# Performance work log

Measured on AMD Instinct MI355X. Metric: run time of the kernel, lower is better.

The kernel has to match this reference:

```python
import jax, jax.numpy as jnp
import numpy as np

B, S, D = 1, 8192, 1024
H, HD = 16, 64
WIN = 1024      # sliding_window_size
CHUNK = 1024    # chunk_size
OVERLAP = 128   # chunk_overlap


def setup_inputs() -> dict:
    key = jax.random.key(0)
    ks = jax.random.split(key, 5)
    s = 1.0 / np.sqrt(D)
    inp = {"x": jax.random.normal(ks[0], (B, S, D), jnp.float32)}
    for i, n in enumerate(["Wq", "Wk", "Wv", "Wo"]):
        inp[n] = jax.random.normal(ks[1 + i], (D, D), jnp.float32) * s
    for n in ["bq", "bk", "bv", "bo"]:
        inp[n] = jnp.zeros((D,), jnp.float32)
    return inp


def _attend_chunk(q, k, v, chunk_start, win_start):
    # q: [B, Lq, H, HD]; k, v: [B, Lk, H, HD]
    Lq, Lk = q.shape[1], k.shape[1]
    q_abs = chunk_start + jnp.arange(Lq)[:, None]   # absolute query positions
    k_abs = win_start + jnp.arange(Lk)[None, :]     # absolute key positions
    allowed = (k_abs >= q_abs - WIN // 2) & (k_abs < q_abs + WIN // 2)
    scale = 1.0 / np.sqrt(HD)
    scores = jnp.einsum('bqhd,bkhd->bhqk', q, k) * scale  # [B,H,Lq,Lk]
    scores = jnp.where(allowed[None, None], scores, -jnp.inf)
    p = jax.nn.softmax(scores, axis=-1)
    return jnp.einsum('bhqk,bkhd->bqhd', p, v)


def _overlap_weight(cs, ce):
    # replicate torch linspace overlap-add blend weights (host-side constants)
    w = np.ones(ce - cs, np.float32)
    if cs > 0:
        n = min(cs + OVERLAP, ce) - cs
        w[:n] = np.linspace(0.0, 1.0, n, dtype=np.float32)
    if ce < S:
        os_ = max(cs, ce - OVERLAP)
        w[os_ - cs:] = np.linspace(1.0, 0.0, ce - os_, dtype=np.float32)
    return jnp.asarray(w)


def reference(x, Wq, bq, Wk, bk, Wv, bv, Wo, bo):
    q = (x @ Wq.T + bq).reshape(B, S, H, HD)
    k = (x @ Wk.T + bk).reshape(B, S, H, HD)
    v = (x @ Wv.T + bv).reshape(B, S, H, HD)
    out = jnp.zeros((B, S, H, HD), x.dtype)
    step = CHUNK - OVERLAP
    for cs in range(0, S, step):  # static Python loop over ~10 chunks
        ce = min(cs + CHUNK, S)
        ws, we = max(0, cs - WIN // 2), min(S, ce + WIN // 2)
        o = _attend_chunk(q[:, cs:ce], k[:, ws:we], v[:, ws:we], cs, ws)
        w = _overlap_weight(cs, ce)
        out = out.at[:, cs:ce].add(o * w[None, :, None, None])
    out = out.reshape(B, S, D)
    return out @ Wo.T + bo
```

## Files before the change

### kernel.cpp

```cpp
#include <hip/hip_runtime.h>

#define DEVI __device__ __forceinline__

constexpr int S = 8192, D = 1024, H = 16, HD = 64;
constexpr int NQKV = 3 * D;

typedef __attribute__((ext_vector_type(8))) __bf16 bf16x8;
typedef __attribute__((ext_vector_type(8))) unsigned short us8;
typedef __attribute__((ext_vector_type(4))) float f32x4;

DEVI unsigned short f2b(float f) {
  unsigned int u = __float_as_uint(f);
  u += 0x7fff + ((u >> 16) & 1);
  return (unsigned short)(u >> 16);
}

DEVI ushort4 cvt4(float4 v) {
  ushort4 r; r.x = f2b(v.x); r.y = f2b(v.y); r.z = f2b(v.z); r.w = f2b(v.w); return r;
}

DEVI void load_lds16(const void* g, void* l) {
  __builtin_amdgcn_global_load_lds((const __attribute__((address_space(1))) void*)g,
                                   (__attribute__((address_space(3))) void*)l,
                                   16, 0, 0);
}

__global__ void prep_kernel(const float4* __restrict__ x,
                            const float4* __restrict__ Wq, const float4* __restrict__ Wk,
                            const float4* __restrict__ Wv, const float4* __restrict__ Wo,
                            const float4* __restrict__ bq, const float4* __restrict__ bk,
                            const float4* __restrict__ bv,
                            ushort4* __restrict__ xb, ushort4* __restrict__ wqkv,
                            ushort4* __restrict__ wob, float4* __restrict__ biasq)
{
  constexpr int NX = S * D / 4;
  constexpr int NW = D * D / 4;
  constexpr int NB = D / 4;
  constexpr int TOT = NX + 4 * NW + 3 * NB;
  for (int i = blockIdx.x * blockDim.x + threadIdx.x; i < TOT; i += gridDim.x * blockDim.x) {
    if (i < NX) {
      xb[i] = cvt4(x[i]);
    } else if (i < NX + 3 * NW) {
      int j = i - NX;
      const float4* src = (j < NW) ? Wq : ((j < 2 * NW) ? Wk : Wv);
      int jj = (j < NW) ? j : ((j < 2 * NW) ? j - NW : j - 2 * NW);
      wqkv[j] = cvt4(src[jj]);
    } else if (i < NX + 4 * NW) {
      int j = i - NX - 3 * NW;
      wob[j] = cvt4(Wo[j]);
    } else {
      int j = i - NX - 4 * NW;
      const float4* src = (j < NB) ? bq : ((j < 2 * NB) ? bk : bv);
      int jj = (j < NB) ? j : ((j < 2 * NB) ? j - NB : j - 2 * NB);
      biasq[j] = src[jj];
    }
  }
}

template<int LDC, bool OUT_BF16>
__global__ __launch_bounds__(256)
void gemm_nt(const unsigned short* __restrict__ A,
             const unsigned short* __restrict__ B,
             const float* __restrict__ bias,
             void* __restrict__ C, int K)
{
  __shared__ __align__(16) unsigned short As[128 * 32];
  __shared__ __align__(16) unsigned short Bs[128 * 32];
  const int tid = threadIdx.x;
  const int wave = tid >> 6, lane = tid & 63;
  const int quad = lane >> 4, l15 = lane & 15;
  const int m0 = blockIdx.x * 128, n0 = blockIdx.y * 128;
  const int wr = wave >> 1, wc = wave & 1;

  const f32x4 fzero = {0.f, 0.f, 0.f, 0.f};
  f32x4 acc[4][4];
#pragma unroll
  for (int i = 0; i < 4; ++i)
#pragma unroll
    for (int j = 0; j < 4; ++j) acc[i][j] = fzero;

  const int segr = lane >> 2;
  const int cpst = lane & 3;

  for (int k0 = 0; k0 < K; k0 += 32) {
    __syncthreads();
#pragma unroll
    for (int j = 0; j < 4; ++j) {
      const int s = wave * 4 + j;
      const int s7 = s & 7;
      const int r = s7 * 16 + segr;
      const int c = cpst ^ ((r >> 1) & 3);
      const unsigned short* g = (s < 8)
        ? A + (size_t)(m0 + r) * K + k0 + c * 8
        : B + (size_t)(n0 + r) * K + k0 + c * 8;
      unsigned short* l = ((s < 8) ? As : Bs) + s7 * 512;
      load_lds16(g, l);
    }
    __syncthreads();

    bf16x8 af[4], bfr[4];
#pragma unroll
    for (int it = 0; it < 4; ++it) {
      const int r = wr * 64 + it * 16 + l15;
      const int cp = quad ^ ((r >> 1) & 3);
      af[it] = *(const bf16x8*)&As[r * 32 + cp * 8];
    }
#pragma unroll
    for (int jt = 0; jt < 4; ++jt) {
      const int r = wc * 64 + jt * 16 + l15;
      const int cp = quad ^ ((r >> 1) & 3);
      bfr[jt] = *(const bf16x8*)&Bs[r * 32 + cp * 8];
    }
#pragma unroll
    for (int it = 0; it < 4; ++it)
#pragma unroll
      for (int jt = 0; jt < 4; ++jt)
        acc[it][jt] = __builtin_amdgcn_mfma_f32_16x16x32_bf16(af[it], bfr[jt], acc[it][jt], 0, 0, 0);
  }

#pragma unroll
  for (int it = 0; it < 4; ++it)
#pragma unroll
    for (int jt = 0; jt < 4; ++jt) {
      const int col = n0 + wc * 64 + jt * 16 + l15;
      const float bv = bias[col];
#pragma unroll
      for (int i = 0; i < 4; ++i) {
        const int row = m0 + wr * 64 + it * 16 + quad * 4 + i;
        const float v = acc[it][jt][i] + bv;
        if constexpr (OUT_BF16)
          ((unsigned short*)C)[(size_t)row * LDC + col] = f2b(v);
        else
          ((float*)C)[(size_t)row * LDC + col] = v;
      }
    }
}

__global__ __launch_bounds__(256)
void attn_fused(const unsigned short* __restrict__ qkv,
                unsigned short* __restrict__ attnb)
{
  __shared__ __align__(16) unsigned short Ks[64 * 64];
  __shared__ __align__(16) unsigned short Vt[64 * 72];
  __shared__ __align__(16) unsigned short Ps[4][2][16 * 72];
  const int tid = threadIdx.x;
  const int wave = tid >> 6, lane = tid & 63;
  const int quad = lane >> 4, l15 = lane & 15;
  const int h = blockIdx.y;
  const int q0 = blockIdx.x * 128;
  const int wq0 = q0 + wave * 32;

  const unsigned short* Qp = qkv + h * HD;
  const unsigned short* Kp = qkv + D + h * HD;
  const unsigned short* Vp = qkv + 2 * D + h * HD;

  bf16x8 qf[2][2];
#pragma unroll
  for (int rt = 0; rt < 2; ++rt)
#pragma unroll
    for (int st = 0; st < 2; ++st)
      qf[rt][st] = *(const bf16x8*)(Qp + (size_t)(wq0 + rt * 16 + l15) * NQKV + st * 32 + quad * 8);

  const f32x4 fzero = {0.f, 0.f, 0.f, 0.f};
  f32x4 o[2][4];
  float lr[2][4];
#pragma unroll
  for (int rt = 0; rt < 2; ++rt)
#pragma unroll
    for (int i = 0; i < 4; ++i) { o[rt][i] = fzero; lr[rt][i] = 0.f; }

  const int ks = (q0 >= 512) ? (q0 - 512) : 0;
  const int ke = (q0 + 640 < S) ? (q0 + 640) : S;

  const int skey = tid >> 3;
  const int sg   = tid & 7;
  const int kdc  = sg ^ (skey & 7);

  for (int kt = ks; kt < ke; kt += 64) {
    __syncthreads();
#pragma unroll
    for (int r = 0; r < 2; ++r) {
      const int key = skey + r * 32;
      load_lds16(Kp + (size_t)(kt + key) * NQKV + kdc * 8, Ks + (size_t)tid * 8 + r * 2048);
    }
#pragma unroll
    for (int r = 0; r < 2; ++r) {
      const int key = skey + r * 32;
      us8 v = *(const us8*)(Vp + (size_t)(kt + key) * NQKV + sg * 8);
      const int ch = (key >> 3) ^ sg;
      unsigned short* dst = Vt + sg * 8 * 72 + ch * 8 + (key & 7);
#pragma unroll
      for (int j = 0; j < 8; ++j) dst[j * 72] = v[j];
    }
    __syncthreads();

    if (kt + 63 >= wq0 - 512 && kt <= wq0 + 542) {
      bf16x8 kf[4][2];
#pragma unroll
      for (int hh = 0; hh < 4; ++hh)
#pragma unroll
        for (int st = 0; st < 2; ++st)
          kf[hh][st] = *(const bf16x8*)&Ks[(hh * 16 + l15) * 64 + ((st * 4 + quad) ^ (l15 & 7)) * 8];

#pragma unroll
      for (int rt = 0; rt < 2; ++rt) {
        const int R = wq0 + rt * 16;
        bool act[2];
#pragma unroll
        for (int st = 0; st < 2; ++st) {
          const int C0 = kt + st * 32;
          act[st] = (C0 + 31 >= R - 512) && (C0 <= R + 526);
        }
        if (!act[0] && !act[1]) continue;
        unsigned short* Pw = (unsigned short*)Ps[wave][rt];

#pragma unroll
        for (int hh = 0; hh < 4; ++hh) {
          if (!act[hh >> 1]) continue;
          const int C = kt + hh * 16;
          const bool any  = (C + 15 >= R - 512) && (C <= R + 526);
          const bool full = (C >= R - 497) && (C <= R + 496);
          float p[4];
          if (!any) {
            p[0] = p[1] = p[2] = p[3] = 0.f;
          } else {
            f32x4 z = fzero;
            z = __builtin_amdgcn_mfma_f32_16x16x32_bf16(qf[rt][0], kf[hh][0], z, 0, 0, 0);
            z = __builtin_amdgcn_mfma_f32_16x16x32_bf16(qf[rt][1], kf[hh][1], z, 0, 0, 0);
            if (full) {
#pragma unroll
              for (int i = 0; i < 4; ++i) p[i] = __expf(z[i] * 0.125f);
            } else {
#pragma unroll
              for (int i = 0; i < 4; ++i) {
                const int qa = R + quad * 4 + i;
                const int ka = C + l15;
                const unsigned u = (unsigned)(ka - qa + 512);
                p[i] = (u < 1024u) ? __expf(z[i] * 0.125f) : 0.f;
              }
            }
          }
#pragma unroll
          for (int i = 0; i < 4; ++i) {
            lr[rt][i] += p[i];
            Pw[(quad * 4 + i) * 72 + hh * 16 + l15] = f2b(p[i]);
          }
        }
        asm volatile("s_waitcnt lgkmcnt(0)" ::: "memory");

#pragma unroll
        for (int st = 0; st < 2; ++st) {
          if (!act[st]) continue;
          const bf16x8 pf = *(const bf16x8*)&Pw[l15 * 72 + (st * 4 + quad) * 8];
#pragma unroll
          for (int vt = 0; vt < 4; ++vt) {
            const int d = vt * 16 + l15;
            const bf16x8 vf = *(const bf16x8*)&Vt[d * 72 + (((st * 4 + quad) ^ (d >> 3)) & 7) * 8
                                                  + ((st * 4 + quad) & ~7) * 8];
            o[rt][vt] = __builtin_amdgcn_mfma_f32_16x16x32_bf16(pf, vf, o[rt][vt], 0, 0, 0);
          }
        }
      }
    }
  }

#pragma unroll
  for (int rt = 0; rt < 2; ++rt)
#pragma unroll
    for (int i = 0; i < 4; ++i) {
      float l = lr[rt][i];
#pragma unroll
      for (int dd = 1; dd < 16; dd <<= 1) l += __shfl_xor(l, dd);
      const int qa = wq0 + rt * 16 + quad * 4 + i;
      const float w = (qa >= S - 128) ? (1.0f + (float)(qa - (S - 128)) * (1.0f / 127.0f)) : 1.0f;
      const float scl = w / l;
#pragma unroll
      for (int vt = 0; vt < 4; ++vt)
        attnb[(size_t)qa * D + h * HD + vt * 16 + l15] = f2b(o[rt][vt][i] * scl);
    }
}

extern "C" void kernel_launch(void* const* d_in, const int* in_sizes, int n_in,
                              void* d_out, int out_size, void* d_ws, size_t ws_size,
                              hipStream_t stream)
{
  const float* x  = (const float*)d_in[0];
  const float* Wq = (const float*)d_in[1];
  const float* Wk = (const float*)d_in[2];
  const float* Wv = (const float*)d_in[3];
  const float* Wo = (const float*)d_in[4];
  const float* bq = (const float*)d_in[5];
  const float* bk = (const float*)d_in[6];
  const float* bv = (const float*)d_in[7];
  const float* bo = (const float*)d_in[8];

  char* ws = (char*)d_ws;
  unsigned short* xb    = (unsigned short*)(ws);
  unsigned short* wqkv  = (unsigned short*)(ws + 16777216);
  unsigned short* wob   = (unsigned short*)(ws + 23068672);
  float*          biasq = (float*)         (ws + 25165824);
  unsigned short* qkv   = (unsigned short*)(ws + 25178112);
  unsigned short* attnb = (unsigned short*)(ws + 75509760);

  prep_kernel<<<2048, 256, 0, stream>>>((const float4*)x, (const float4*)Wq, (const float4*)Wk,
                                        (const float4*)Wv, (const float4*)Wo, (const float4*)bq,
                                        (const float4*)bk, (const float4*)bv,
                                        (ushort4*)xb, (ushort4*)wqkv, (ushort4*)wob, (float4*)biasq);

  gemm_nt<NQKV, true><<<dim3(64, 24), 256, 0, stream>>>(xb, wqkv, biasq, (void*)qkv, D);
  attn_fused<<<dim3(S / 128, H), 256, 0, stream>>>(qkv, attnb);
  gemm_nt<D, false><<<dim3(64, 8), 256, 0, stream>>>(attnb, wob, bo, d_out, D);
}
```

Before: 313.9 us.

## Double-buffer K/V tiles in attention and reorder loop to share K/V fragments across rows

The attention kernel now double-buffers the K and V LDS tiles. The next tile's K is staged asynchronously and its V is held in registers while the current tile is computed, and V is scattered into the other buffer only after compute, so one barrier per iteration is removed. The inner loops are reordered so each 32-key slice loads K and V fragments once and reuses them for both row tiles, which also shrinks the per-wave P buffer. The cost is double the K/V LDS footprint and more live registers, which may lower occupancy.

```diff
diff --git a/kernel.cpp b/kernel.cpp
--- a/kernel.cpp
+++ b/kernel.cpp
@@ -140,9 +140,9 @@
 void attn_fused(const unsigned short* __restrict__ qkv,
                 unsigned short* __restrict__ attnb)
 {
-  __shared__ __align__(16) unsigned short Ks[64 * 64];
-  __shared__ __align__(16) unsigned short Vt[64 * 72];
-  __shared__ __align__(16) unsigned short Ps[4][2][16 * 72];
+  __shared__ __align__(16) unsigned short Ks[2][64 * 64];
+  __shared__ __align__(16) unsigned short Vt[2][64 * 72];
+  __shared__ __align__(16) unsigned short Ps[4][16 * 72];
   const int tid = threadIdx.x;
   const int wave = tid >> 6, lane = tid & 63;
   const int quad = lane >> 4, l15 = lane & 15;
@@ -158,8 +158,8 @@
 #pragma unroll
   for (int rt = 0; rt < 2; ++rt)
 #pragma unroll
-    for (int st = 0; st < 2; ++st)
-      qf[rt][st] = *(const bf16x8*)(Qp + (size_t)(wq0 + rt * 16 + l15) * NQKV + st * 32 + quad * 8);
+    for (int ksp = 0; ksp < 2; ++ksp)
+      qf[rt][ksp] = *(const bf16x8*)(Qp + (size_t)(wq0 + rt * 16 + l15) * NQKV + ksp * 32 + quad * 8);
 
   const f32x4 fzero = {0.f, 0.f, 0.f, 0.f};
   f32x4 o[2][4];
@@ -176,92 +176,112 @@
   const int sg   = tid & 7;
   const int kdc  = sg ^ (skey & 7);
 
-  for (int kt = ks; kt < ke; kt += 64) {
+  us8 vreg[2];
+
+#define STAGE_K(kt_, b_)                                                          \
+  {                                                                               \
+    _Pragma("unroll")                                                             \
+    for (int r = 0; r < 2; ++r)                                                   \
+      load_lds16(Kp + (size_t)((kt_) + skey + r * 32) * NQKV + kdc * 8,           \
+                 &Ks[b_][(size_t)tid * 8 + r * 2048]);                            \
+  }
+#define LOAD_V(kt_)                                                               \
+  {                                                                               \
+    _Pragma("unroll")                                                             \
+    for (int r = 0; r < 2; ++r)                                                   \
+      vreg[r] = *(const us8*)(Vp + (size_t)((kt_) + skey + r * 32) * NQKV + sg * 8); \
+  }
+#define SCAT_V(b_)                                                                \
+  {                                                                               \
+    _Pragma("unroll")                                                             \
+    for (int r = 0; r < 2; ++r) {                                                 \
+      const int key = skey + r * 32;                                              \
+      const int ch = (key >> 3) ^ sg;                                             \
+      unsigned short* dst = &Vt[b_][sg * 8 * 72 + ch * 8 + (key & 7)];            \
+      _Pragma("unroll")                                                           \
+      for (int j = 0; j < 8; ++j) dst[j * 72] = vreg[r][j];                       \
+    }                                                                             \
+  }
+
+  STAGE_K(ks, 0);
+  LOAD_V(ks);
+  SCAT_V(0);
+
+  int b = 0;
+  for (int kt = ks; kt < ke; kt += 64, b ^= 1) {
     __syncthreads();
-#pragma unroll
-    for (int r = 0; r < 2; ++r) {
-      const int key = skey + r * 32;
-      load_lds16(Kp + (size_t)(kt + key) * NQKV + kdc * 8, Ks + (size_t)tid * 8 + r * 2048);
-    }
-#pragma unroll
-    for (int r = 0; r < 2; ++r) {
-      const int key = skey + r * 32;
-      us8 v = *(const us8*)(Vp + (size_t)(kt + key) * NQKV + sg * 8);
-      const int ch = (key >> 3) ^ sg;
-      unsigned short* dst = Vt + sg * 8 * 72 + ch * 8 + (key & 7);
-#pragma unroll
-      for (int j = 0; j < 8; ++j) dst[j * 72] = v[j];
-    }
-    __syncthreads();
+    const int nx = kt + 64;
+    const bool more = (nx < ke);
+    if (more) { STAGE_K(nx, b ^ 1); LOAD_V(nx); }
 
     if (kt + 63 >= wq0 - 512 && kt <= wq0 + 542) {
-      bf16x8 kf[4][2];
-#pragma unroll
-      for (int hh = 0; hh < 4; ++hh)
-#pragma unroll
-        for (int st = 0; st < 2; ++st)
-          kf[hh][st] = *(const bf16x8*)&Ks[(hh * 16 + l15) * 64 + ((st * 4 + quad) ^ (l15 & 7)) * 8];
-
-#pragma unroll
-      for (int rt = 0; rt < 2; ++rt) {
-        const int R = wq0 + rt * 16;
-        bool act[2];
-#pragma unroll
-        for (int st = 0; st < 2; ++st) {
-          const int C0 = kt + st * 32;
-          act[st] = (C0 + 31 >= R - 512) && (C0 <= R + 526);
+      unsigned short* Pw = (unsigned short*)Ps[wave];
+#pragma unroll
+      for (int st = 0; st < 2; ++st) {
+        const int C0 = kt + st * 32;
+        if (!((C0 + 31 >= wq0 - 512) && (C0 <= wq0 + 16 + 526))) continue;
+
+        bf16x8 kf[2][2];
+#pragma unroll
+        for (int hh2 = 0; hh2 < 2; ++hh2)
+#pragma unroll
+          for (int ksp = 0; ksp < 2; ++ksp)
+            kf[hh2][ksp] = *(const bf16x8*)&Ks[b][((st * 2 + hh2) * 16 + l15) * 64
+                                                  + ((ksp * 4 + quad) ^ (l15 & 7)) * 8];
+        bf16x8 vf[4];
+#pragma unroll
+        for (int vt = 0; vt < 4; ++vt) {
+          const int d = vt * 16 + l15;
+          vf[vt] = *(const bf16x8*)&Vt[b][d * 72 + (((st * 4 + quad) ^ (d >> 3)) & 7) * 8];
         }
-        if (!act[0] && !act[1]) continue;
-        unsigned short* Pw = (unsigned short*)Ps[wave][rt];
-
-#pragma unroll
-        for (int hh = 0; hh < 4; ++hh) {
-          if (!act[hh >> 1]) continue;
-          const int C = kt + hh * 16;
-          const bool any  = (C + 15 >= R - 512) && (C <= R + 526);
-          const bool full = (C >= R - 497) && (C <= R + 496);
-          float p[4];
-          if (!any) {
-            p[0] = p[1] = p[2] = p[3] = 0.f;
-          } else {
-            f32x4 z = fzero;
-            z = __builtin_amdgcn_mfma_f32_16x16x32_bf16(qf[rt][0], kf[hh][0], z, 0, 0, 0);
-            z = __builtin_amdgcn_mfma_f32_16x16x32_bf16(qf[rt][1], kf[hh][1], z, 0, 0, 0);
-            if (full) {
-#pragma unroll
-              for (int i = 0; i < 4; ++i) p[i] = __expf(z[i] * 0.125f);
+
+#pragma unroll
+        for (int rt = 0; rt < 2; ++rt) {
+          const int R = wq0 + rt * 16;
+          if (!((C0 + 31 >= R - 512) && (C0 <= R + 526))) continue;
+
+#pragma unroll
+          for (int hh2 = 0; hh2 < 2; ++hh2) {
+            const int C = C0 + hh2 * 16;
+            const bool any  = (C + 15 >= R - 512) && (C <= R + 526);
+            const bool full = (C >= R - 497) && (C <= R + 496);
+            float p[4];
+            if (!any) {
+              p[0] = p[1] = p[2] = p[3] = 0.f;
             } else {
-#pragma unroll
-              for (int i = 0; i < 4; ++i) {
-                const int qa = R + quad * 4 + i;
-                const int ka = C + l15;
-                const unsigned u = (unsigned)(ka - qa + 512);
-                p[i] = (u < 1024u) ? __expf(z[i] * 0.125f) : 0.f;
+              f32x4 z = fzero;
+              z = __builtin_amdgcn_mfma_f32_16x16x32_bf16(qf[rt][0], kf[hh2][0], z, 0, 0, 0);
+              z = __builtin_amdgcn_mfma_f32_16x16x32_bf16(qf[rt][1], kf[hh2][1], z, 0, 0, 0);
+              if (full) {
+#pragma unroll
+                for (int i = 0; i < 4; ++i) p[i] = __expf(z[i] * 0.125f);
+              } else {
+#pragma unroll
+                for (int i = 0; i < 4; ++i) {
+                  const int qa = R + quad * 4 + i;
+                  const int ka = C + l15;
+                  const unsigned u = (unsigned)(ka - qa + 512);
+                  p[i] = (u < 1024u) ? __expf(z[i] * 0.125f) : 0.f;
+                }
               }
             }
+#pragma unroll
+            for (int i = 0; i < 4; ++i) {
+              lr[rt][i] += p[i];
+              Pw[(quad * 4 + i) * 72 + st * 32 + hh2 * 16 + l15] = f2b(p[i]);
+            }
           }
-#pragma unroll
-          for (int i = 0; i < 4; ++i) {
-            lr[rt][i] += p[i];
-            Pw[(quad * 4 + i) * 72 + hh * 16 + l15] = f2b(p[i]);
-          }
-        }
-        asm volatile("s_waitcnt lgkmcnt(0)" ::: "memory");
-
-#pragma unroll
-        for (int st = 0; st < 2; ++st) {
-          if (!act[st]) continue;
+          asm volatile("s_waitcnt lgkmcnt(0)" ::: "memory");
+
           const bf16x8 pf = *(const bf16x8*)&Pw[l15 * 72 + (st * 4 + quad) * 8];
 #pragma unroll
-          for (int vt = 0; vt < 4; ++vt) {
-            const int d = vt * 16 + l15;
-            const bf16x8 vf = *(const bf16x8*)&Vt[d * 72 + (((st * 4 + quad) ^ (d >> 3)) & 7) * 8
-                                                  + ((st * 4 + quad) & ~7) * 8];
-            o[rt][vt] = __builtin_amdgcn_mfma_f32_16x16x32_bf16(pf, vf, o[rt][vt], 0, 0, 0);
-          }
+          for (int vt = 0; vt < 4; ++vt)
+            o[rt][vt] = __builtin_amdgcn_mfma_f32_16x16x32_bf16(pf, vf[vt], o[rt][vt], 0, 0, 0);
         }
       }
     }
+
+    if (more) SCAT_V(b ^ 1);
   }
 
 #pragma unroll
@@ -278,6 +298,9 @@
       for (int vt = 0; vt < 4; ++vt)
         attnb[(size_t)qa * D + h * HD + vt * 16 + l15] = f2b(o[rt][vt][i] * scl);
     }
+#undef STAGE_K
+#undef LOAD_V
+#undef SCAT_V
 }
 
 extern "C" void kernel_launch(void* const* d_in, const int* in_sizes, int n_in,
```

Result: faster. 304.8 us (-2.9%).
